# Kernel tuning notes

Measured on AMD Instinct MI355X. Metric: run time of the kernel, lower is better.

Reference implementation:

```python
import jax, jax.numpy as jnp
import numpy as np

N = 8192
E = 131072
C_IN = 256
C_OUT = 256


def setup_inputs() -> dict:
    key = jax.random.key(0)
    k1, k2, k3, k4 = jax.random.split(key, 4)
    x = jax.random.normal(k1, (N, C_IN), dtype=jnp.float32)
    edge_index = jax.random.randint(k2, (2, E), 0, N, dtype=jnp.int64)
    # nn.Linear params (PyTorch layout: W is (out, in))
    bound = 1.0 / np.sqrt(C_IN)
    W = jax.random.uniform(k3, (C_OUT, C_IN), minval=-bound, maxval=bound, dtype=jnp.float32)
    b_lin = jax.random.uniform(k4, (C_OUT,), minval=-bound, maxval=bound, dtype=jnp.float32)
    bias = jnp.zeros((C_OUT,), dtype=jnp.float32)  # extra learned bias parameter
    return {"x": x, "W": W, "b_lin": b_lin, "bias": bias, "edge_index": edge_index}


def reference(x, W, b_lin, bias, edge_index):
    n = x.shape[0]
    # Dense adjacency built by scatter ASSIGNMENT (duplicate edges collapse to 1.0),
    # matching torch's adj[e0, e1] = 1.0
    adj = jnp.zeros((n, n), dtype=x.dtype).at[edge_index[0], edge_index[1]].set(1.0)
    # adj = adj + eye (diagonal entries can become 2.0 if self-loop edge exists)
    diag = jnp.arange(n)
    adj = adj.at[diag, diag].add(1.0)
    deg = adj.sum(axis=1)
    # pow(deg, -0.5) with inf -> 0 (deg == 0 case)
    deg_inv_sqrt = jnp.where(deg > 0, 1.0 / jnp.sqrt(deg), 0.0)
    # symmetric normalization: D^-1/2 A D^-1/2
    norm = deg_inv_sqrt[:, None] * adj * deg_inv_sqrt[None, :]
    out = norm @ x                      # (N, C_in)
    out = out @ W.T + b_lin + bias      # (N, C_out)
    return out
```

## Files before the change

### kernel.cpp

```cpp
#include <hip/hip_runtime.h>
#include <stdint.h>

#define N_NODES 8192
#define CH      256
#define NWORDS  256
#define BM_WORDS (N_NODES * NWORDS)

typedef short bf16x8 __attribute__((ext_vector_type(8)));
typedef float f32x4  __attribute__((ext_vector_type(4)));

static __device__ __forceinline__ unsigned short f2bf(float f) {
    union { float f; uint32_t u; } v; v.f = f;
    uint32_t r = v.u + 0x7fff + ((v.u >> 16) & 1);
    return (unsigned short)(r >> 16);
}

__global__ void k_init(uint32_t* __restrict__ bm) {
    int i = blockIdx.x * blockDim.x + threadIdx.x;
    if (i < BM_WORDS) bm[i] = 0u;
}

__global__ void k_edges(const int* __restrict__ ei, uint32_t* __restrict__ bm, int E) {
    int e = blockIdx.x * blockDim.x + threadIdx.x;
    if (e >= E) return;
    int r = ei[e];
    int c = ei[E + e];
    atomicOr(&bm[r * NWORDS + (c >> 5)], 1u << (c & 31));
}

__global__ __launch_bounds__(64) void k_degree(const uint32_t* __restrict__ bm,
                                               float* __restrict__ dis) {
    int row  = blockIdx.x;
    int lane = threadIdx.x;
    const uint4* p = (const uint4*)(bm + row * NWORDS);
    uint4 w = p[lane];
    int cnt = __popc(w.x) + __popc(w.y) + __popc(w.z) + __popc(w.w);
    for (int off = 32; off; off >>= 1) cnt += __shfl_down(cnt, off);
    if (lane == 0) dis[row] = rsqrtf((float)(cnt + 1));
}

__global__ void k_convW(const float* __restrict__ W, unsigned short* __restrict__ Wb) {
    int i = blockIdx.x * blockDim.x + threadIdx.x;
    if (i < CH * CH) Wb[i] = f2bf(W[i]);
}

__global__ __launch_bounds__(256) void k_aggregate(const uint32_t* __restrict__ bm,
                                                   const float* __restrict__ x,
                                                   const float* __restrict__ dis,
                                                   unsigned short* __restrict__ out1) {
    int row = blockIdx.x;
    int t   = threadIdx.x;
    __shared__ unsigned short s_list[N_NODES];
    __shared__ int s_cnt;
    if (t == 0) s_cnt = 0;
    __syncthreads();

    uint32_t w = bm[row * NWORDS + t];
    while (w) {
        int b = __ffs(w) - 1;
        int pos = atomicAdd(&s_cnt, 1);
        s_list[pos] = (unsigned short)(t * 32 + b);
        w &= (w - 1);
    }
    __syncthreads();

    int cnt = s_cnt;
    float di = dis[row];
    float acc = di * x[row * CH + t];
    for (int k = 0; k < cnt; ++k) {
        int j = s_list[k];
        acc += dis[j] * x[j * CH + t];
    }
    out1[row * CH + t] = f2bf(di * acc);
}

__global__ __launch_bounds__(256) void k_gemm_mfma(const unsigned short* __restrict__ A,
                                                   const unsigned short* __restrict__ Wb,
                                                   const float* __restrict__ b1,
                                                   const float* __restrict__ b2,
                                                   float* __restrict__ out) {
    int wave = threadIdx.x >> 6;
    int lane = threadIdx.x & 63;
    int m16  = lane & 15;
    int quad = lane >> 4;
    int rowBase = blockIdx.x * 64 + wave * 16;
    int colBase = blockIdx.y * 64;

    f32x4 acc[4] = {};
    const unsigned short* arow = A + (size_t)(rowBase + m16) * CH + quad * 8;

    #pragma unroll
    for (int k0 = 0; k0 < CH; k0 += 32) {
        bf16x8 af = *(const bf16x8*)(arow + k0);
        #pragma unroll
        for (int t = 0; t < 4; ++t) {
            const unsigned short* wrow = Wb + (size_t)(colBase + t * 16 + m16) * CH + quad * 8 + k0;
            bf16x8 bfr = *(const bf16x8*)wrow;
            acc[t] = __builtin_amdgcn_mfma_f32_16x16x32_bf16(af, bfr, acc[t], 0, 0, 0);
        }
    }

    #pragma unroll
    for (int t = 0; t < 4; ++t) {
        int col = colBase + t * 16 + m16;
        float bb = b1[col] + b2[col];
        #pragma unroll
        for (int r = 0; r < 4; ++r) {
            int row = rowBase + quad * 4 + r;
            out[(size_t)row * CH + col] = acc[t][r] + bb;
        }
    }
}

extern "C" void kernel_launch(void* const* d_in, const int* in_sizes, int n_in,
                              void* d_out, int out_size, void* d_ws, size_t ws_size,
                              hipStream_t stream) {
    const float* x     = (const float*)d_in[0];
    const float* W     = (const float*)d_in[1];
    const float* b_lin = (const float*)d_in[2];
    const float* bias  = (const float*)d_in[3];
    const int*   ei    = (const int*)d_in[4];
    int E = in_sizes[4] / 2;
    float* out = (float*)d_out;

    uint8_t* ws = (uint8_t*)d_ws;
    uint32_t*       bm  = (uint32_t*)ws;
    float*          dis = (float*)(ws + (size_t)BM_WORDS * 4);
    unsigned short* o1  = (unsigned short*)(ws + (size_t)BM_WORDS * 4 + 32 * 1024);
    unsigned short* Wb  = (unsigned short*)(ws + (size_t)BM_WORDS * 4 + 32 * 1024 + (size_t)N_NODES * CH * 2);

    k_init<<<(BM_WORDS + 255) / 256, 256, 0, stream>>>(bm);
    k_edges<<<(E + 255) / 256, 256, 0, stream>>>(ei, bm, E);
    k_degree<<<N_NODES, 64, 0, stream>>>(bm, dis);
    k_convW<<<(CH * CH + 255) / 256, 256, 0, stream>>>(W, Wb);
    k_aggregate<<<N_NODES, 256, 0, stream>>>(bm, x, dis, o1);
    dim3 gg(N_NODES / 64, CH / 64);
    k_gemm_mfma<<<gg, 256, 0, stream>>>(o1, Wb, b_lin, bias, out);
}
```

Before: 112.0 us.

## Pre-scale x into bf16 y and gather bf16 rows with 64-thread aggregate

A new pass computes each row's degree and stores y = dis*x in bf16; it also converts W to bf16 in the same launch. Aggregation then gathers half-size bf16 rows with 4-wide vectorized loads per lane, 64 threads per row, and no per-neighbor dis lookup. Rows are read four neighbours at a time for memory-level parallelism. k_init is replaced by hipMemsetAsync. The risk is lower accuracy from rounding the pre-scaled inputs to bf16 before summation.

```diff
diff --git a/kernel.cpp b/kernel.cpp
--- a/kernel.cpp
+++ b/kernel.cpp
@@ -14,10 +14,14 @@
     uint32_t r = v.u + 0x7fff + ((v.u >> 16) & 1);
     return (unsigned short)(r >> 16);
 }
-
-__global__ void k_init(uint32_t* __restrict__ bm) {
-    int i = blockIdx.x * blockDim.x + threadIdx.x;
-    if (i < BM_WORDS) bm[i] = 0u;
+static __device__ __forceinline__ uint32_t pack2bf(float lo, float hi) {
+    return (uint32_t)f2bf(lo) | ((uint32_t)f2bf(hi) << 16);
+}
+static __device__ __forceinline__ float bfbits_lo(uint32_t u) {
+    union { uint32_t u; float f; } v; v.u = u << 16; return v.f;
+}
+static __device__ __forceinline__ float bfbits_hi(uint32_t u) {
+    union { uint32_t u; float f; } v; v.u = u & 0xffff0000u; return v.f;
 }
 
 __global__ void k_edges(const int* __restrict__ ei, uint32_t* __restrict__ bm, int E) {
@@ -28,50 +32,92 @@
     atomicOr(&bm[r * NWORDS + (c >> 5)], 1u << (c & 31));
 }
 
-__global__ __launch_bounds__(64) void k_degree(const uint32_t* __restrict__ bm,
-                                               float* __restrict__ dis) {
+__global__ __launch_bounds__(64) void k_deg_y(const uint32_t* __restrict__ bm,
+                                              const float* __restrict__ x,
+                                              const float* __restrict__ W,
+                                              uint32_t* __restrict__ y,
+                                              uint32_t* __restrict__ Wb) {
+    int lane = threadIdx.x;
+    if (blockIdx.x < N_NODES) {
+        int row = blockIdx.x;
+        uint4 w4 = ((const uint4*)(bm + row * NWORDS))[lane];
+        int cnt = __popc(w4.x) + __popc(w4.y) + __popc(w4.z) + __popc(w4.w);
+        #pragma unroll
+        for (int off = 1; off < 64; off <<= 1) cnt += __shfl_xor(cnt, off);
+        float di = rsqrtf((float)(cnt + 1));
+        float4 xv = ((const float4*)(x + (size_t)row * CH))[lane];
+        uint2 o;
+        o.x = pack2bf(di * xv.x, di * xv.y);
+        o.y = pack2bf(di * xv.z, di * xv.w);
+        ((uint2*)y)[row * 64 + lane] = o;
+    } else {
+        int i = (blockIdx.x - N_NODES) * 256 + lane * 4;
+        float4 wv = *(const float4*)(W + i);
+        uint2 o;
+        o.x = pack2bf(wv.x, wv.y);
+        o.y = pack2bf(wv.z, wv.w);
+        *(uint2*)(Wb + i / 2) = o;
+    }
+}
+
+__global__ __launch_bounds__(64) void k_aggregate(const uint32_t* __restrict__ bm,
+                                                  const uint32_t* __restrict__ y,
+                                                  uint32_t* __restrict__ o1) {
     int row  = blockIdx.x;
     int lane = threadIdx.x;
-    const uint4* p = (const uint4*)(bm + row * NWORDS);
-    uint4 w = p[lane];
-    int cnt = __popc(w.x) + __popc(w.y) + __popc(w.z) + __popc(w.w);
-    for (int off = 32; off; off >>= 1) cnt += __shfl_down(cnt, off);
-    if (lane == 0) dis[row] = rsqrtf((float)(cnt + 1));
-}
-
-__global__ void k_convW(const float* __restrict__ W, unsigned short* __restrict__ Wb) {
-    int i = blockIdx.x * blockDim.x + threadIdx.x;
-    if (i < CH * CH) Wb[i] = f2bf(W[i]);
-}
-
-__global__ __launch_bounds__(256) void k_aggregate(const uint32_t* __restrict__ bm,
-                                                   const float* __restrict__ x,
-                                                   const float* __restrict__ dis,
-                                                   unsigned short* __restrict__ out1) {
-    int row = blockIdx.x;
-    int t   = threadIdx.x;
-    __shared__ unsigned short s_list[N_NODES];
+    __shared__ __align__(16) unsigned short s_list[N_NODES];
     __shared__ int s_cnt;
-    if (t == 0) s_cnt = 0;
+    if (lane == 0) s_cnt = 0;
     __syncthreads();
 
-    uint32_t w = bm[row * NWORDS + t];
-    while (w) {
-        int b = __ffs(w) - 1;
-        int pos = atomicAdd(&s_cnt, 1);
-        s_list[pos] = (unsigned short)(t * 32 + b);
-        w &= (w - 1);
+    uint4 w4 = ((const uint4*)(bm + row * NWORDS))[lane];
+    int my = __popc(w4.x) + __popc(w4.y) + __popc(w4.z) + __popc(w4.w);
+    uint32_t wrd[4] = {w4.x, w4.y, w4.z, w4.w};
+    #pragma unroll
+    for (int i = 0; i < 4; ++i) {
+        uint32_t w = wrd[i];
+        int basebit = lane * 128 + i * 32;
+        while (w) {
+            int b = __ffs(w) - 1;
+            int p = atomicAdd(&s_cnt, 1);
+            s_list[p] = (unsigned short)(basebit + b);
+            w &= (w - 1);
+        }
     }
+    #pragma unroll
+    for (int off = 1; off < 64; off <<= 1) my += __shfl_xor(my, off);
+    float di = rsqrtf((float)(my + 1));
     __syncthreads();
+    int cnt = s_cnt;
 
-    int cnt = s_cnt;
-    float di = dis[row];
-    float acc = di * x[row * CH + t];
-    for (int k = 0; k < cnt; ++k) {
+    const uint2* ys = (const uint2*)y;
+    uint2 d = ys[row * 64 + lane];
+    float a0 = bfbits_lo(d.x), a1 = bfbits_hi(d.x);
+    float a2 = bfbits_lo(d.y), a3 = bfbits_hi(d.y);
+
+    int k = 0;
+    for (; k + 4 <= cnt; k += 4) {
+        ushort4 js = *(const ushort4*)&s_list[k];
+        uint2 d0 = ys[(int)js.x * 64 + lane];
+        uint2 d1 = ys[(int)js.y * 64 + lane];
+        uint2 d2 = ys[(int)js.z * 64 + lane];
+        uint2 d3 = ys[(int)js.w * 64 + lane];
+        a0 += bfbits_lo(d0.x); a1 += bfbits_hi(d0.x); a2 += bfbits_lo(d0.y); a3 += bfbits_hi(d0.y);
+        a0 += bfbits_lo(d1.x); a1 += bfbits_hi(d1.x); a2 += bfbits_lo(d1.y); a3 += bfbits_hi(d1.y);
+        a0 += bfbits_lo(d2.x); a1 += bfbits_hi(d2.x); a2 += bfbits_lo(d2.y); a3 += bfbits_hi(d2.y);
+        a0 += bfbits_lo(d3.x); a1 += bfbits_hi(d3.x); a2 += bfbits_lo(d3.y); a3 += bfbits_hi(d3.y);
+    }
+    for (; k < cnt; ++k) {
         int j = s_list[k];
-        acc += dis[j] * x[j * CH + t];
+        uint2 dd = ys[j * 64 + lane];
+        a0 += bfbits_lo(dd.x); a1 += bfbits_hi(dd.x);
+        a2 += bfbits_lo(dd.y); a3 += bfbits_hi(dd.y);
     }
-    out1[row * CH + t] = f2bf(di * acc);
+
+    uint2 o;
+    o.x = pack2bf(di * a0, di * a1);
+    o.y = pack2bf(di * a2, di * a3);
+    ((uint2*)o1)[row * 64 + lane] = o;
 }
 
 __global__ __launch_bounds__(256) void k_gemm_mfma(const unsigned short* __restrict__ A,
@@ -124,16 +170,16 @@
     float* out = (float*)d_out;
 
     uint8_t* ws = (uint8_t*)d_ws;
-    uint32_t*       bm  = (uint32_t*)ws;
-    float*          dis = (float*)(ws + (size_t)BM_WORDS * 4);
-    unsigned short* o1  = (unsigned short*)(ws + (size_t)BM_WORDS * 4 + 32 * 1024);
-    unsigned short* Wb  = (unsigned short*)(ws + (size_t)BM_WORDS * 4 + 32 * 1024 + (size_t)N_NODES * CH * 2);
+    uint32_t* bm = (uint32_t*)ws;
+    uint32_t* y  = (uint32_t*)(ws + (8u << 20));
+    uint32_t* o1 = (uint32_t*)(ws + (12u << 20));
+    uint32_t* Wb = (uint32_t*)(ws + (16u << 20));
 
-    k_init<<<(BM_WORDS + 255) / 256, 256, 0, stream>>>(bm);
+    hipMemsetAsync(bm, 0, (size_t)BM_WORDS * 4, stream);
     k_edges<<<(E + 255) / 256, 256, 0, stream>>>(ei, bm, E);
-    k_degree<<<N_NODES, 64, 0, stream>>>(bm, dis);
-    k_convW<<<(CH * CH + 255) / 256, 256, 0, stream>>>(W, Wb);
-    k_aggregate<<<N_NODES, 256, 0, stream>>>(bm, x, dis, o1);
+    k_deg_y<<<N_NODES + 256, 64, 0, stream>>>(bm, x, W, y, Wb);
+    k_aggregate<<<N_NODES, 64, 0, stream>>>(bm, y, o1);
     dim3 gg(N_NODES / 64, CH / 64);
-    k_gemm_mfma<<<gg, 256, 0, stream>>>(o1, Wb, b_lin, bias, out);
+    k_gemm_mfma<<<gg, 256, 0, stream>>>((const unsigned short*)o1, (const unsigned short*)Wb,
+                                        b_lin, bias, out);
 }
```

New measurement: 107.0 us. 4.5% less time.
